# Kernel optimization log

Hardware: AMD Instinct MI355X
Metric: run time of the kernel (lower is better)

Reference implementation:

```python
import jax, jax.numpy as jnp
import numpy as np

RADIUS = 1.0 / 16.0
MAX_NEIGHBORS = 64  # forward() passes max_num_neighbors=64
N_POINTS = 16384
N_CLOUDS = 8


def _radius_neighbors(pos, batch, r, k):
    """Dense radius graph: for each point, up to k in-radius same-cloud neighbors.
    Returns idx [N,k] int32 and mask [N,k] bool. loop=True -> self always valid."""
    sq = jnp.sum(pos * pos, axis=-1)                        # [N]
    d2 = sq[:, None] + sq[None, :] - 2.0 * (pos @ pos.T)    # [N,N]
    d2 = jnp.maximum(d2, 0.0)
    valid = (d2 <= r * r) & (batch[:, None] == batch[None, :])
    score = jnp.where(valid, -d2, -jnp.inf)
    vals, idx = jax.lax.top_k(score, k)                     # nearest-first, [N,k]
    mask = vals > -jnp.inf
    return idx, mask


def _point_conv(x, pos, idx, mask, W1, b1, W2, b2):
    """PointNetConv: msg = relu(Linear([x_j, pos_j - pos_i])), max-agg, Linear."""
    xj = x[idx]                                   # [N,K,c_in]  gather
    rel = pos[idx] - pos[:, None, :]              # [N,K,3]
    h = jnp.concatenate([xj, rel], axis=-1) @ W1 + b1   # [N,K,c_mid]
    h = jax.nn.relu(h)
    h = jnp.where(mask[..., None], h, -jnp.inf)
    agg = jnp.max(h, axis=1)                      # [N,c_mid]  max aggregation
    agg = jnp.where(jnp.isfinite(agg), agg, 0.0)  # safety (loop=True makes this moot)
    return agg @ W2 + b2                          # [N,c_out]


def setup_inputs() -> dict:
    key = jax.random.key(0)
    ks = jax.random.split(key, 16)
    pos = jax.random.uniform(ks[0], (N_POINTS, 3), dtype=jnp.float32)
    rgb = jax.random.uniform(ks[1], (N_POINTS, 3), dtype=jnp.float32)
    batch = jnp.sort(jax.random.randint(ks[2], (N_POINTS,), 0, N_CLOUDS)).astype(jnp.int64)

    def lin(k, fan_in, fan_out):
        kw, kb = jax.random.split(k)
        bound = 1.0 / np.sqrt(fan_in)
        W = jax.random.uniform(kw, (fan_in, fan_out), jnp.float32, -bound, bound)
        b = jax.random.uniform(kb, (fan_out,), jnp.float32, -bound, bound)
        return W, b

    W1a, b1a = lin(ks[3], 3 + 3, 8)
    W2a, b2a = lin(ks[4], 8, 8)
    W1b, b1b = lin(ks[5], 8 + 3, 16)
    W2b, b2b = lin(ks[6], 16, 16)
    W1c, b1c = lin(ks[7], 16 + 3, 32)
    W2c, b2c = lin(ks[8], 32, 32)
    return {"pos": pos, "rgb": rgb, "batch": batch,
            "W1a": W1a, "b1a": b1a, "W2a": W2a, "b2a": b2a,
            "W1b": W1b, "b1b": b1b, "W2b": W2b, "b2b": b2b,
            "W1c": W1c, "b1c": b1c, "W2c": W2c, "b2c": b2c}


def reference(pos, rgb, batch,
              W1a, b1a, W2a, b2a,
              W1b, b1b, W2b, b2b,
              W1c, b1c, W2c, b2c):
    # NOTE: rgb is accepted by the original forward() but never used.
    idx, mask = _radius_neighbors(pos, batch, RADIUS, MAX_NEIGHBORS)
    out = jax.nn.celu(_point_conv(pos, pos, idx, mask, W1a, b1a, W2a, b2a))
    out = jax.nn.celu(_point_conv(out, pos, idx, mask, W1b, b1b, W2b, b2b))
    out = jax.nn.celu(_point_conv(out, pos, idx, mask, W1c, b1c, W2c, b2c))
    return pos, out, batch
```

## Files before the change

kernel.cpp:

```cpp
#include <hip/hip_runtime.h>
#include <math.h>

#define N_POINTS 16384
#define CELLS_PER_CLOUD 4096
#define N_CELLS 32768
#define CAP 16
#define NBR_STRIDE 32

constexpr double R2D = 1.0 / 256.0;

__global__ __launch_bounds__(256) void k_prep(const float* __restrict__ pos,
                                              const int* __restrict__ batch,
                                              float* __restrict__ out,
                                              int* __restrict__ cnt,
                                              float4* __restrict__ bucket,
                                              float4* __restrict__ pos4)
{
    int i = blockIdx.x * 256 + threadIdx.x;
    out[i]                = pos[i];
    out[i + N_POINTS]     = pos[i + N_POINTS];
    out[i + 2 * N_POINTS] = pos[i + 2 * N_POINTS];
    out[3 * N_POINTS + 32 * N_POINTS + i] = (float)batch[i];

    float x = pos[3 * i], y = pos[3 * i + 1], z = pos[3 * i + 2];
    int ix = min(max((int)(x * 16.f), 0), 15);
    int iy = min(max((int)(y * 16.f), 0), 15);
    int iz = min(max((int)(z * 16.f), 0), 15);
    int cell = ((batch[i] * 16 + iz) * 16 + iy) * 16 + ix;
    pos4[i] = make_float4(x, y, z, __int_as_float(cell));
    int slot = atomicAdd(&cnt[cell], 1);
    if (slot < CAP) bucket[cell * CAP + slot] = make_float4(x, y, z, __int_as_float(i));
}

__global__ __launch_bounds__(512) void k_search_a(
    const float4* __restrict__ pos4,
    const int* __restrict__ cnt, const float4* __restrict__ bucket,
    const float* __restrict__ W1, const float* __restrict__ b1,
    const float* __restrict__ W2, const float* __restrict__ b2,
    float* __restrict__ out_a, float4* __restrict__ nbr, int* __restrict__ nbr_cnt)
{
    __shared__ float sW1[48], sB1[8], sW2[64], sB2[8];
    __shared__ float4 s_hits[NBR_STRIDE][64];
    __shared__ int s_k[64];

    int t = threadIdx.x;
    int p = t & 63;
    int g = t >> 6;

    if (t < 48) sW1[t] = W1[t];
    if (t < 8) { sB1[t] = b1[t]; sB2[t] = b2[t]; }
    if (t < 64) { sW2[t] = W2[t]; s_k[t] = 0; }
    __syncthreads();

    int i = blockIdx.x * 64 + p;
    float4 pi4 = pos4[i];
    float xi = pi4.x, yi = pi4.y, zi = pi4.z;
    double xd = (double)xi, yd = (double)yi, zd = (double)zi;
    int cell0 = __float_as_int(pi4.w);
    int ix = cell0 & 15, iy = (cell0 >> 4) & 15, iz = (cell0 >> 8) & 15;
    int cb = cell0 & ~(CELLS_PER_CLOUD - 1);

    int n[4], cid[4];
#pragma unroll
    for (int cc = 0; cc < 4; cc++) {
        int c = g + 8 * cc;
        int dz = c / 9 - 1, dy = (c / 3) % 3 - 1, dx = c % 3 - 1;
        int zz = iz + dz, yy = iy + dy, xx = ix + dx;
        bool ok = (c < 27) & ((zz | yy | xx) >= 0) & (zz < 16) & (yy < 16) & (xx < 16);
        int zc = min(max(zz, 0), 15), yc = min(max(yy, 0), 15),
            xc = min(max(xx, 0), 15);
        cid[cc] = cb + (zc << 8) + (yc << 4) + xc;
        int nc = min(cnt[cid[cc]], CAP);
        n[cc] = ok ? nc : 0;
    }
    int nmax = 0;
#pragma unroll
    for (int cc = 0; cc < 4; cc++) nmax = max(nmax, n[cc]);

    for (int s = 0; s < nmax; s++) {
#pragma unroll
        for (int cc = 0; cc < 4; cc++) {
            if (s < n[cc]) {
                float4 q = bucket[cid[cc] * CAP + s];
                double ddx = xd - (double)q.x, ddy = yd - (double)q.y,
                       ddz = zd - (double)q.z;
                double d2 = ddx * ddx + ddy * ddy + ddz * ddz;
                if (d2 <= R2D) {
                    int slot = atomicAdd(&s_k[p], 1);
                    if (slot < NBR_STRIDE) {
                        s_hits[slot][p] = q;
                        nbr[i * NBR_STRIDE + slot] = q;
                    }
                }
            }
        }
    }
    __syncthreads();

    if (g == 0) {
        int kc = min(s_k[p], NBR_STRIDE);
        nbr_cnt[i] = kc;

        float mx[8];
#pragma unroll
        for (int m = 0; m < 8; m++) mx[m] = 0.f;
        for (int kk = 0; kk < kc; kk++) {
            float4 q = s_hits[kk][p];
            float in6[6] = { q.x, q.y, q.z, q.x - xi, q.y - yi, q.z - zi };
#pragma unroll
            for (int m = 0; m < 8; m++) {
                float h = sB1[m];
#pragma unroll
                for (int c6 = 0; c6 < 6; c6++) h = fmaf(in6[c6], sW1[c6 * 8 + m], h);
                mx[m] = fmaxf(mx[m], fmaxf(h, 0.f));
            }
        }

        float o[8];
#pragma unroll
        for (int m = 0; m < 8; m++) {
            float v = sB2[m];
#pragma unroll
            for (int kk = 0; kk < 8; kk++) v = fmaf(mx[kk], sW2[kk * 8 + m], v);
            o[m] = v > 0.f ? v : expm1f(v);
        }
        *(float4*)&out_a[i * 8]     = make_float4(o[0], o[1], o[2], o[3]);
        *(float4*)&out_a[i * 8 + 4] = make_float4(o[4], o[5], o[6], o[7]);
    }
}

template<int CIN4, int CMID, int PTS>
__global__ __launch_bounds__(256) void k_conv(
    const float4* __restrict__ pos4, const float4* __restrict__ xin4,
    const float4* __restrict__ nbr, const int* __restrict__ nbr_cnt,
    const float* __restrict__ W1, const float* __restrict__ b1,
    const float* __restrict__ W2, const float* __restrict__ b2,
    float* __restrict__ xout)
{
    constexpr int CIN = CIN4 * 4;
    __shared__ float s_agg[PTS * CMID];
    int p = threadIdx.x / CMID;
    int m = threadIdx.x % CMID;
    int i = blockIdx.x * PTS + p;

    float4 pi = pos4[i];
    int cnt = nbr_cnt[i];

    float w1c[CIN + 3];
#pragma unroll
    for (int k = 0; k < CIN + 3; k++) w1c[k] = W1[k * CMID + m];
    float w2c[CMID];
#pragma unroll
    for (int k = 0; k < CMID; k++) w2c[k] = W2[k * CMID + m];
    float bb = b1[m];

    float mxv = 0.f;
    for (int t = 0; t < cnt; t++) {
        float4 q = nbr[i * NBR_STRIDE + t];
        int j = __float_as_int(q.w);
        float h = bb;
#pragma unroll
        for (int k = 0; k < CIN4; k++) {
            float4 v = xin4[j * CIN4 + k];
            h = fmaf(v.x, w1c[4 * k],     h);
            h = fmaf(v.y, w1c[4 * k + 1], h);
            h = fmaf(v.z, w1c[4 * k + 2], h);
            h = fmaf(v.w, w1c[4 * k + 3], h);
        }
        h = fmaf(q.x - pi.x, w1c[CIN],     h);
        h = fmaf(q.y - pi.y, w1c[CIN + 1], h);
        h = fmaf(q.z - pi.z, w1c[CIN + 2], h);
        mxv = fmaxf(mxv, fmaxf(h, 0.f));
    }
    s_agg[p * CMID + m] = mxv;
    __syncthreads();

    float o = b2[m];
#pragma unroll
    for (int k = 0; k < CMID; k++) o = fmaf(s_agg[p * CMID + k], w2c[k], o);
    xout[i * CMID + m] = o > 0.f ? o : expm1f(o);
}

extern "C" void kernel_launch(void* const* d_in, const int* in_sizes, int n_in,
                              void* d_out, int out_size, void* d_ws, size_t ws_size,
                              hipStream_t stream)
{
    const float* pos   = (const float*)d_in[0];
    const int*   batch = (const int*)d_in[2];
    const float* W1a = (const float*)d_in[3];
    const float* b1a = (const float*)d_in[4];
    const float* W2a = (const float*)d_in[5];
    const float* b2a = (const float*)d_in[6];
    const float* W1b = (const float*)d_in[7];
    const float* b1b = (const float*)d_in[8];
    const float* W2b = (const float*)d_in[9];
    const float* b2b = (const float*)d_in[10];
    const float* W1c = (const float*)d_in[11];
    const float* b1c = (const float*)d_in[12];
    const float* W2c = (const float*)d_in[13];
    const float* b2c = (const float*)d_in[14];

    float* out = (float*)d_out;

    char* ws = (char*)d_ws;
    size_t off = 0;
    auto alloc = [&](size_t bytes) {
        char* p = ws + off; off += (bytes + 255) & ~size_t(255); return p;
    };
    int*    cnt     = (int*)alloc(N_CELLS * 4);
    float4* bucket  = (float4*)alloc((size_t)N_CELLS * CAP * 16);
    float4* pos4    = (float4*)alloc(N_POINTS * 16);
    int*    nbr_cnt = (int*)alloc(N_POINTS * 4);
    float4* nbr     = (float4*)alloc((size_t)N_POINTS * NBR_STRIDE * 16);
    float*  out_a   = (float*)alloc(N_POINTS * 8 * 4);
    float*  out_b   = (float*)alloc(N_POINTS * 16 * 4);

    hipMemsetAsync(cnt, 0, N_CELLS * 4, stream);
    hipLaunchKernelGGL(k_prep, dim3(N_POINTS / 256), dim3(256), 0, stream,
                       pos, batch, out, cnt, bucket, pos4);
    hipLaunchKernelGGL(k_search_a, dim3(N_POINTS / 64), dim3(512), 0, stream,
                       pos4, cnt, bucket, W1a, b1a, W2a, b2a,
                       out_a, nbr, nbr_cnt);
    hipLaunchKernelGGL((k_conv<2, 16, 16>), dim3(N_POINTS / 16), dim3(256), 0, stream,
                       pos4, (const float4*)out_a, nbr, nbr_cnt,
                       W1b, b1b, W2b, b2b, out_b);
    hipLaunchKernelGGL((k_conv<4, 32, 8>), dim3(N_POINTS / 8), dim3(256), 0, stream,
                       pos4, (const float4*)out_b, nbr, nbr_cnt,
                       W1c, b1c, W2c, b2c, out + 3 * N_POINTS);
}
```

Measured before the change: 117.3 us.

## Fuse all stages into one cooperative persistent kernel with grid syncs

Replaces the memset, prep, search and two conv kernels with a single cooperative kernel of 256 blocks of 512 threads, with grid.sync between phases. Each block keeps its points' neighbor lists in shared memory across all three convolution layers, so the global nbr/nbr_cnt buffers are no longer written and re-read. The first layer's per-point MLP is spread across all 8 thread groups instead of one, and the three layers' weights are staged in shared memory. In exchange it adds four grid-wide barriers and uses more shared memory and registers per block, which can limit residency and costs some parallelism in the conv stages, which now run 64 points per block.

```diff
diff --git a/kernel.cpp b/kernel.cpp
--- a/kernel.cpp
+++ b/kernel.cpp
@@ -1,58 +1,78 @@
 #include <hip/hip_runtime.h>
+#include <hip/hip_cooperative_groups.h>
 #include <math.h>
+
+namespace cg = cooperative_groups;
 
 #define N_POINTS 16384
 #define CELLS_PER_CLOUD 4096
 #define N_CELLS 32768
 #define CAP 16
 #define NBR_STRIDE 32
+#define TPB 512
+#define NBLK (N_POINTS / 64)
 
 constexpr double R2D = 1.0 / 256.0;
 
-__global__ __launch_bounds__(256) void k_prep(const float* __restrict__ pos,
-                                              const int* __restrict__ batch,
-                                              float* __restrict__ out,
-                                              int* __restrict__ cnt,
-                                              float4* __restrict__ bucket,
-                                              float4* __restrict__ pos4)
+__global__ __launch_bounds__(TPB) void k_mega(
+    const float* __restrict__ pos, const int* __restrict__ batch,
+    const float* __restrict__ W1a, const float* __restrict__ b1a,
+    const float* __restrict__ W2a, const float* __restrict__ b2a,
+    const float* __restrict__ W1b, const float* __restrict__ b1b,
+    const float* __restrict__ W2b, const float* __restrict__ b2b,
+    const float* __restrict__ W1c, const float* __restrict__ b1c,
+    const float* __restrict__ W2c, const float* __restrict__ b2c,
+    float* __restrict__ out, int* __restrict__ cnt,
+    float4* __restrict__ bucket, float4* __restrict__ pos4,
+    float* __restrict__ out_a, float* __restrict__ out_b)
 {
-    int i = blockIdx.x * 256 + threadIdx.x;
-    out[i]                = pos[i];
-    out[i + N_POINTS]     = pos[i + N_POINTS];
-    out[i + 2 * N_POINTS] = pos[i + 2 * N_POINTS];
-    out[3 * N_POINTS + 32 * N_POINTS + i] = (float)batch[i];
-
-    float x = pos[3 * i], y = pos[3 * i + 1], z = pos[3 * i + 2];
-    int ix = min(max((int)(x * 16.f), 0), 15);
-    int iy = min(max((int)(y * 16.f), 0), 15);
-    int iz = min(max((int)(z * 16.f), 0), 15);
-    int cell = ((batch[i] * 16 + iz) * 16 + iy) * 16 + ix;
-    pos4[i] = make_float4(x, y, z, __int_as_float(cell));
-    int slot = atomicAdd(&cnt[cell], 1);
-    if (slot < CAP) bucket[cell * CAP + slot] = make_float4(x, y, z, __int_as_float(i));
-}
-
-__global__ __launch_bounds__(512) void k_search_a(
-    const float4* __restrict__ pos4,
-    const int* __restrict__ cnt, const float4* __restrict__ bucket,
-    const float* __restrict__ W1, const float* __restrict__ b1,
-    const float* __restrict__ W2, const float* __restrict__ b2,
-    float* __restrict__ out_a, float4* __restrict__ nbr, int* __restrict__ nbr_cnt)
-{
-    __shared__ float sW1[48], sB1[8], sW2[64], sB2[8];
+    cg::grid_group grid = cg::this_grid();
+
+    __shared__ float sW1a[48], sB1a[8], sW2a[64], sB2a[8];
+    __shared__ float sW1b[11 * 16], sB1b[16], sW2b[16 * 16], sB2b[16];
+    __shared__ float sW1c[19 * 32], sB1c[32], sW2c[32 * 32], sB2c[32];
     __shared__ float4 s_hits[NBR_STRIDE][64];
-    __shared__ int s_k[64];
-
-    int t = threadIdx.x;
+    __shared__ int   s_k[64];
+    __shared__ float s_mx[64][9];
+    __shared__ float s_aggb[64][17];
+    __shared__ float s_aggc[64][33];
+
+    int t = threadIdx.x, b = blockIdx.x;
     int p = t & 63;
     int g = t >> 6;
 
-    if (t < 48) sW1[t] = W1[t];
-    if (t < 8) { sB1[t] = b1[t]; sB2[t] = b2[t]; }
-    if (t < 64) { sW2[t] = W2[t]; s_k[t] = 0; }
-    __syncthreads();
-
-    int i = blockIdx.x * 64 + p;
+    if (t < 48) sW1a[t] = W1a[t];
+    if (t < 8)  { sB1a[t] = b1a[t]; sB2a[t] = b2a[t]; }
+    if (t < 64) { sW2a[t] = W2a[t]; s_k[t] = 0; }
+    if (t < 176) sW1b[t] = W1b[t];
+    if (t < 256) sW2b[t] = W2b[t];
+    if (t < 16) { sB1b[t] = b1b[t]; sB2b[t] = b2b[t]; }
+    for (int k = t; k < 608;  k += TPB) sW1c[k] = W1c[k];
+    for (int k = t; k < 1024; k += TPB) sW2c[k] = W2c[k];
+    if (t < 32) { sB1c[t] = b1c[t]; sB2c[t] = b2c[t]; }
+
+    if (t < 128) cnt[b * 128 + t] = 0;
+    if (t < 192) { int idx = b * 192 + t; out[idx] = pos[idx]; }
+    if (t < 64) {
+        int i = b * 64 + t;
+        out[3 * N_POINTS + 32 * N_POINTS + i] = (float)batch[i];
+    }
+    grid.sync();
+
+    if (t < 64) {
+        int i = b * 64 + t;
+        float x = pos[3 * i], y = pos[3 * i + 1], z = pos[3 * i + 2];
+        int ix = min(max((int)(x * 16.f), 0), 15);
+        int iy = min(max((int)(y * 16.f), 0), 15);
+        int iz = min(max((int)(z * 16.f), 0), 15);
+        int cell = ((batch[i] * 16 + iz) * 16 + iy) * 16 + ix;
+        pos4[i] = make_float4(x, y, z, __int_as_float(cell));
+        int slot = atomicAdd(&cnt[cell], 1);
+        if (slot < CAP) bucket[cell * CAP + slot] = make_float4(x, y, z, __int_as_float(i));
+    }
+    grid.sync();
+
+    int i = b * 64 + p;
     float4 pi4 = pos4[i];
     float xi = pi4.x, yi = pi4.y, zi = pi4.z;
     double xd = (double)xi, yd = (double)yi, zd = (double)zi;
@@ -87,98 +107,138 @@
                 double d2 = ddx * ddx + ddy * ddy + ddz * ddz;
                 if (d2 <= R2D) {
                     int slot = atomicAdd(&s_k[p], 1);
-                    if (slot < NBR_STRIDE) {
-                        s_hits[slot][p] = q;
-                        nbr[i * NBR_STRIDE + slot] = q;
-                    }
+                    if (slot < NBR_STRIDE) s_hits[slot][p] = q;
                 }
             }
         }
     }
     __syncthreads();
-
-    if (g == 0) {
-        int kc = min(s_k[p], NBR_STRIDE);
-        nbr_cnt[i] = kc;
-
-        float mx[8];
-#pragma unroll
-        for (int m = 0; m < 8; m++) mx[m] = 0.f;
+    int kc = min(s_k[p], NBR_STRIDE);
+
+    {
+        float mxv = 0.f;
         for (int kk = 0; kk < kc; kk++) {
             float4 q = s_hits[kk][p];
             float in6[6] = { q.x, q.y, q.z, q.x - xi, q.y - yi, q.z - zi };
-#pragma unroll
-            for (int m = 0; m < 8; m++) {
-                float h = sB1[m];
-#pragma unroll
-                for (int c6 = 0; c6 < 6; c6++) h = fmaf(in6[c6], sW1[c6 * 8 + m], h);
-                mx[m] = fmaxf(mx[m], fmaxf(h, 0.f));
+            float h = sB1a[g];
+#pragma unroll
+            for (int c6 = 0; c6 < 6; c6++) h = fmaf(in6[c6], sW1a[c6 * 8 + g], h);
+            mxv = fmaxf(mxv, fmaxf(h, 0.f));
+        }
+        s_mx[p][g] = mxv;
+    }
+    __syncthreads();
+    {
+        float o = sB2a[g];
+#pragma unroll
+        for (int k = 0; k < 8; k++) o = fmaf(s_mx[p][k], sW2a[k * 8 + g], o);
+        out_a[i * 8 + g] = o > 0.f ? o : expm1f(o);
+    }
+    grid.sync();
+
+    {
+        const float4* xa = (const float4*)out_a;
+        int m0 = g, m1 = g + 8;
+        float w0[11], w1[11];
+#pragma unroll
+        for (int k = 0; k < 11; k++) { w0[k] = sW1b[k * 16 + m0]; w1[k] = sW1b[k * 16 + m1]; }
+        float bb0 = sB1b[m0], bb1 = sB1b[m1];
+        float mx0 = 0.f, mx1 = 0.f;
+        for (int kk = 0; kk < kc; kk++) {
+            float4 q = s_hits[kk][p];
+            int j = __float_as_int(q.w);
+            float4 v0 = xa[j * 2], v1 = xa[j * 2 + 1];
+            float rx = q.x - xi, ry = q.y - yi, rz = q.z - zi;
+            float h0 = bb0, h1 = bb1;
+            h0 = fmaf(v0.x, w0[0], h0); h1 = fmaf(v0.x, w1[0], h1);
+            h0 = fmaf(v0.y, w0[1], h0); h1 = fmaf(v0.y, w1[1], h1);
+            h0 = fmaf(v0.z, w0[2], h0); h1 = fmaf(v0.z, w1[2], h1);
+            h0 = fmaf(v0.w, w0[3], h0); h1 = fmaf(v0.w, w1[3], h1);
+            h0 = fmaf(v1.x, w0[4], h0); h1 = fmaf(v1.x, w1[4], h1);
+            h0 = fmaf(v1.y, w0[5], h0); h1 = fmaf(v1.y, w1[5], h1);
+            h0 = fmaf(v1.z, w0[6], h0); h1 = fmaf(v1.z, w1[6], h1);
+            h0 = fmaf(v1.w, w0[7], h0); h1 = fmaf(v1.w, w1[7], h1);
+            h0 = fmaf(rx, w0[8],  h0);  h1 = fmaf(rx, w1[8],  h1);
+            h0 = fmaf(ry, w0[9],  h0);  h1 = fmaf(ry, w1[9],  h1);
+            h0 = fmaf(rz, w0[10], h0);  h1 = fmaf(rz, w1[10], h1);
+            mx0 = fmaxf(mx0, fmaxf(h0, 0.f));
+            mx1 = fmaxf(mx1, fmaxf(h1, 0.f));
+        }
+        s_aggb[p][m0] = mx0;
+        s_aggb[p][m1] = mx1;
+        __syncthreads();
+        float o0 = sB2b[m0], o1 = sB2b[m1];
+#pragma unroll
+        for (int k = 0; k < 16; k++) {
+            float a = s_aggb[p][k];
+            o0 = fmaf(a, sW2b[k * 16 + m0], o0);
+            o1 = fmaf(a, sW2b[k * 16 + m1], o1);
+        }
+        out_b[i * 16 + m0] = o0 > 0.f ? o0 : expm1f(o0);
+        out_b[i * 16 + m1] = o1 > 0.f ? o1 : expm1f(o1);
+    }
+    grid.sync();
+
+    {
+        const float4* xb = (const float4*)out_b;
+        float w1[4][19];
+#pragma unroll
+        for (int cc = 0; cc < 4; cc++) {
+            int mm = g + 8 * cc;
+#pragma unroll
+            for (int k = 0; k < 19; k++) w1[cc][k] = sW1c[k * 32 + mm];
+        }
+        float mx[4] = {0.f, 0.f, 0.f, 0.f};
+        for (int kk = 0; kk < kc; kk++) {
+            float4 q = s_hits[kk][p];
+            int j = __float_as_int(q.w);
+            float4 v0 = xb[j * 4], v1 = xb[j * 4 + 1],
+                   v2 = xb[j * 4 + 2], v3 = xb[j * 4 + 3];
+            float rx = q.x - xi, ry = q.y - yi, rz = q.z - zi;
+#pragma unroll
+            for (int cc = 0; cc < 4; cc++) {
+                float h = sB1c[g + 8 * cc];
+                h = fmaf(v0.x, w1[cc][0],  h);
+                h = fmaf(v0.y, w1[cc][1],  h);
+                h = fmaf(v0.z, w1[cc][2],  h);
+                h = fmaf(v0.w, w1[cc][3],  h);
+                h = fmaf(v1.x, w1[cc][4],  h);
+                h = fmaf(v1.y, w1[cc][5],  h);
+                h = fmaf(v1.z, w1[cc][6],  h);
+                h = fmaf(v1.w, w1[cc][7],  h);
+                h = fmaf(v2.x, w1[cc][8],  h);
+                h = fmaf(v2.y, w1[cc][9],  h);
+                h = fmaf(v2.z, w1[cc][10], h);
+                h = fmaf(v2.w, w1[cc][11], h);
+                h = fmaf(v3.x, w1[cc][12], h);
+                h = fmaf(v3.y, w1[cc][13], h);
+                h = fmaf(v3.z, w1[cc][14], h);
+                h = fmaf(v3.w, w1[cc][15], h);
+                h = fmaf(rx, w1[cc][16], h);
+                h = fmaf(ry, w1[cc][17], h);
+                h = fmaf(rz, w1[cc][18], h);
+                mx[cc] = fmaxf(mx[cc], fmaxf(h, 0.f));
             }
         }
-
-        float o[8];
-#pragma unroll
-        for (int m = 0; m < 8; m++) {
-            float v = sB2[m];
-#pragma unroll
-            for (int kk = 0; kk < 8; kk++) v = fmaf(mx[kk], sW2[kk * 8 + m], v);
-            o[m] = v > 0.f ? v : expm1f(v);
-        }
-        *(float4*)&out_a[i * 8]     = make_float4(o[0], o[1], o[2], o[3]);
-        *(float4*)&out_a[i * 8 + 4] = make_float4(o[4], o[5], o[6], o[7]);
-    }
-}
-
-template<int CIN4, int CMID, int PTS>
-__global__ __launch_bounds__(256) void k_conv(
-    const float4* __restrict__ pos4, const float4* __restrict__ xin4,
-    const float4* __restrict__ nbr, const int* __restrict__ nbr_cnt,
-    const float* __restrict__ W1, const float* __restrict__ b1,
-    const float* __restrict__ W2, const float* __restrict__ b2,
-    float* __restrict__ xout)
-{
-    constexpr int CIN = CIN4 * 4;
-    __shared__ float s_agg[PTS * CMID];
-    int p = threadIdx.x / CMID;
-    int m = threadIdx.x % CMID;
-    int i = blockIdx.x * PTS + p;
-
-    float4 pi = pos4[i];
-    int cnt = nbr_cnt[i];
-
-    float w1c[CIN + 3];
-#pragma unroll
-    for (int k = 0; k < CIN + 3; k++) w1c[k] = W1[k * CMID + m];
-    float w2c[CMID];
-#pragma unroll
-    for (int k = 0; k < CMID; k++) w2c[k] = W2[k * CMID + m];
-    float bb = b1[m];
-
-    float mxv = 0.f;
-    for (int t = 0; t < cnt; t++) {
-        float4 q = nbr[i * NBR_STRIDE + t];
-        int j = __float_as_int(q.w);
-        float h = bb;
-#pragma unroll
-        for (int k = 0; k < CIN4; k++) {
-            float4 v = xin4[j * CIN4 + k];
-            h = fmaf(v.x, w1c[4 * k],     h);
-            h = fmaf(v.y, w1c[4 * k + 1], h);
-            h = fmaf(v.z, w1c[4 * k + 2], h);
-            h = fmaf(v.w, w1c[4 * k + 3], h);
-        }
-        h = fmaf(q.x - pi.x, w1c[CIN],     h);
-        h = fmaf(q.y - pi.y, w1c[CIN + 1], h);
-        h = fmaf(q.z - pi.z, w1c[CIN + 2], h);
-        mxv = fmaxf(mxv, fmaxf(h, 0.f));
-    }
-    s_agg[p * CMID + m] = mxv;
-    __syncthreads();
-
-    float o = b2[m];
-#pragma unroll
-    for (int k = 0; k < CMID; k++) o = fmaf(s_agg[p * CMID + k], w2c[k], o);
-    xout[i * CMID + m] = o > 0.f ? o : expm1f(o);
+#pragma unroll
+        for (int cc = 0; cc < 4; cc++) s_aggc[p][g + 8 * cc] = mx[cc];
+        __syncthreads();
+        float o[4];
+#pragma unroll
+        for (int cc = 0; cc < 4; cc++) o[cc] = sB2c[g + 8 * cc];
+#pragma unroll
+        for (int k = 0; k < 32; k++) {
+            float a = s_aggc[p][k];
+#pragma unroll
+            for (int cc = 0; cc < 4; cc++)
+                o[cc] = fmaf(a, sW2c[k * 32 + g + 8 * cc], o[cc]);
+        }
+#pragma unroll
+        for (int cc = 0; cc < 4; cc++) {
+            float v = o[cc];
+            out[3 * N_POINTS + i * 32 + g + 8 * cc] = v > 0.f ? v : expm1f(v);
+        }
+    }
 }
 
 extern "C" void kernel_launch(void* const* d_in, const int* in_sizes, int n_in,
@@ -210,21 +270,15 @@
     int*    cnt     = (int*)alloc(N_CELLS * 4);
     float4* bucket  = (float4*)alloc((size_t)N_CELLS * CAP * 16);
     float4* pos4    = (float4*)alloc(N_POINTS * 16);
-    int*    nbr_cnt = (int*)alloc(N_POINTS * 4);
-    float4* nbr     = (float4*)alloc((size_t)N_POINTS * NBR_STRIDE * 16);
     float*  out_a   = (float*)alloc(N_POINTS * 8 * 4);
     float*  out_b   = (float*)alloc(N_POINTS * 16 * 4);
 
-    hipMemsetAsync(cnt, 0, N_CELLS * 4, stream);
-    hipLaunchKernelGGL(k_prep, dim3(N_POINTS / 256), dim3(256), 0, stream,
-                       pos, batch, out, cnt, bucket, pos4);
-    hipLaunchKernelGGL(k_search_a, dim3(N_POINTS / 64), dim3(512), 0, stream,
-                       pos4, cnt, bucket, W1a, b1a, W2a, b2a,
-                       out_a, nbr, nbr_cnt);
-    hipLaunchKernelGGL((k_conv<2, 16, 16>), dim3(N_POINTS / 16), dim3(256), 0, stream,
-                       pos4, (const float4*)out_a, nbr, nbr_cnt,
-                       W1b, b1b, W2b, b2b, out_b);
-    hipLaunchKernelGGL((k_conv<4, 32, 8>), dim3(N_POINTS / 8), dim3(256), 0, stream,
-                       pos4, (const float4*)out_b, nbr, nbr_cnt,
-                       W1c, b1c, W2c, b2c, out + 3 * N_POINTS);
+    void* args[] = { (void*)&pos, (void*)&batch,
+                     (void*)&W1a, (void*)&b1a, (void*)&W2a, (void*)&b2a,
+                     (void*)&W1b, (void*)&b1b, (void*)&W2b, (void*)&b2b,
+                     (void*)&W1c, (void*)&b1c, (void*)&W2c, (void*)&b2c,
+                     (void*)&out, (void*)&cnt, (void*)&bucket, (void*)&pos4,
+                     (void*)&out_a, (void*)&out_b };
+    hipLaunchCooperativeKernel((const void*)k_mega, dim3(NBLK), dim3(TPB),
+                               args, 0, stream);
 }
```

Measured after the change: 242.2 us. 106% more time.
